# Optimization experiments

Measured on AMD Instinct MI355X. Metric: run time of the kernel, lower is better.

Reference implementation:

```python
import jax, jax.numpy as jnp
import numpy as np
import math

TPE_DIM = 16
NEG_INF = -1e9


def temporal_positional_encoding(t, dim=TPE_DIM):
    # t: (B, S) continuous positions -> (B, S, dim) sinusoidal encoding
    half = dim // 2
    div_term = jnp.exp(jnp.arange(half, dtype=t.dtype) * (-math.log(10000.0) / dim) * 2.0)
    ang = t[..., None] * div_term  # (B, S, half)
    # interleave sin/cos: pe[..., 0::2]=sin, pe[..., 1::2]=cos
    pe = jnp.stack([jnp.sin(ang), jnp.cos(ang)], axis=-1)  # (B, S, half, 2)
    return pe.reshape(t.shape[0], t.shape[1], dim)


def setup_inputs() -> dict:
    key = jax.random.key(0)
    k1, k2, k3, k4 = jax.random.split(key, 4)
    B, P, S, D = 8, 32, 512, 64
    t = jax.random.uniform(k1, (B, S), dtype=jnp.float32)
    x = jax.random.normal(k2, (B, P, S, D), dtype=jnp.float32)
    mask = jax.random.randint(k3, (B, P, S), 0, 2).astype(jnp.float32)
    # nn.Linear(1,1) weight (only the weight is used in forward)
    alpha_w = jax.random.normal(k4, (1, 1), dtype=jnp.float32) * 0.1
    return {"t": t, "x": x, "mask": mask, "alpha_w": alpha_w}


def reference(t, x, mask, alpha_w):
    B, P, S, D = x.shape
    dk = jnp.float32(TPE_DIM)
    # max-min normalize t over the time dim
    t_min = jnp.min(t, axis=1, keepdims=True)
    t_max = jnp.max(t, axis=1, keepdims=True)
    tn = (t - t_min) / (t_max - t_min)
    # scale by (elu(alpha*1000, 1) + 1)
    scale = jax.nn.elu(alpha_w[0, 0] * 1000.0) + 1.0
    tn = scale * tn
    tpe = temporal_positional_encoding(tn)  # (B, S, TPE_DIM)
    # attention scores over time: (B, S, S), shared across p
    scores = jnp.einsum('bsd,btd->bst', tpe, tpe) / jnp.sqrt(dk)
    eye = jnp.eye(S, dtype=mask.dtype)
    # cond True where (mask_broadcast + eye) < 0.5 -> fill with -1e9
    cond = (mask[:, :, None, :] + eye[None, None, :, :]) < 0.5  # (B, P, S, S)
    sc = jnp.where(cond, jnp.float32(NEG_INF), scores[:, None, :, :])
    p_attn = jax.nn.softmax(sc, axis=-1)  # (B, P, S, S)
    inter_x = jnp.einsum('bpst,bptd->bpsd', p_attn, x)  # (B, P, S, D)
    m = mask[..., None]  # (B, P, S, 1)
    return x * m + inter_x * (1.0 - m)
```

## Files before the change

### kernel.cpp

```cpp
#include <hip/hip_runtime.h>
#include <math.h>

#define B_ 8
#define P_ 32
#define S_ 512
#define D_ 64
#define NQS 5
#define KC 64

typedef __attribute__((ext_vector_type(8))) short short8;
typedef __attribute__((ext_vector_type(4))) float f32x4;

static __device__ inline unsigned short f2bf(float f) {
    unsigned u = __float_as_uint(f);
    unsigned r = (u + 0x7FFFu + ((u >> 16) & 1u)) >> 16;
    return (unsigned short)r;
}
static __device__ inline float bf2f(unsigned short s) {
    return __uint_as_float(((unsigned)s) << 16);
}

__launch_bounds__(256)
__global__ void k_scoresE2(const float* __restrict__ t, const float* __restrict__ alpha_w,
                           unsigned short* __restrict__ E16) {
    const int b = blockIdx.y;
    const int r0 = blockIdx.x * 8;
    const int tid = threadIdx.x, lane = tid & 63, wave = tid >> 6;

    __shared__ float tpeT[16][S_];
    __shared__ float red[8];

    float v0 = t[b * S_ + tid];
    float v1 = t[b * S_ + tid + 256];
    float mn = fminf(v0, v1), mx = fmaxf(v0, v1);
#pragma unroll
    for (int o = 32; o > 0; o >>= 1) {
        mn = fminf(mn, __shfl_xor(mn, o, 64));
        mx = fmaxf(mx, __shfl_xor(mx, o, 64));
    }
    if (lane == 0) { red[wave] = mn; red[4 + wave] = mx; }
    __syncthreads();
    mn = fminf(fminf(red[0], red[1]), fminf(red[2], red[3]));
    mx = fmaxf(fmaxf(red[4], red[5]), fmaxf(red[6], red[7]));

    float aw = alpha_w[0] * 1000.0f;
    float el = aw > 0.0f ? aw : (__expf(aw) - 1.0f);
    float inv = (el + 1.0f) / (mx - mn);

    const float divs[8] = {1.0f, 0.31622776601683794f, 0.1f, 0.031622776601683791f,
                           0.01f, 0.0031622776601683794f, 0.001f, 0.00031622776601683794f};
    {
        float tn0 = (v0 - mn) * inv;
        float tn1 = (v1 - mn) * inv;
#pragma unroll
        for (int f = 0; f < 8; f++) {
            float a0 = tn0 * divs[f], a1 = tn1 * divs[f];
            tpeT[2 * f][tid]           = 0.5f * __sinf(a0);
            tpeT[2 * f + 1][tid]       = 0.5f * __cosf(a0);
            tpeT[2 * f][tid + 256]     = 0.5f * __sinf(a1);
            tpeT[2 * f + 1][tid + 256] = 0.5f * __cosf(a1);
        }
    }
    __syncthreads();

    const int ra = r0 + wave * 2, rb = ra + 1;
    float qa[16], qb[16];
#pragma unroll
    for (int f = 0; f < 16; f++) { qa[f] = tpeT[f][ra]; qb[f] = tpeT[f][rb]; }

    unsigned* Ea = (unsigned*)(E16 + ((size_t)(b * S_) + ra) * S_);
    unsigned* Eb = (unsigned*)(E16 + ((size_t)(b * S_) + rb) * S_);
#pragma unroll
    for (int j = 0; j < 4; j++) {
        int k0 = j * 128 + lane * 2;
        float a0 = 0.f, a1 = 0.f, b0 = 0.f, b1 = 0.f;
#pragma unroll
        for (int f = 0; f < 16; f++) {
            float2 kv = *(const float2*)&tpeT[f][k0];
            a0 += qa[f] * kv.x; a1 += qa[f] * kv.y;
            b0 += qb[f] * kv.x; b1 += qb[f] * kv.y;
        }
        unsigned ea0 = f2bf(__expf(a0 - 2.0f)), ea1 = f2bf(__expf(a1 - 2.0f));
        unsigned eb0 = f2bf(__expf(b0 - 2.0f)), eb1 = f2bf(__expf(b1 - 2.0f));
        Ea[j * 64 + lane] = ea0 | (ea1 << 16);
        Eb[j * 64 + lane] = eb0 | (eb1 << 16);
    }
}

__launch_bounds__(256, 5)
__global__ void k_attn5(const float* __restrict__ x, const float* __restrict__ mask,
                        const unsigned short* __restrict__ E16, float* __restrict__ out) {
    const int bid = blockIdx.x;
    const int b = bid & 7;
    const int rdec = bid >> 3;
    const int p = rdec & 31;
    const int q = rdec >> 5;
    const int bp = b * P_ + p;
    const int tid = threadIdx.x, lane = tid & 63, wave = tid >> 6;
    const int quad = lane >> 4, nlane = lane & 15;
    const int c64 = tid & 63, kg = tid >> 6;

    __shared__ float maskL[S_];
    __shared__ short kidxL[S_], qidxL[S_];
    __shared__ int cntS[2];
    __shared__ __align__(16) unsigned short Bfrag[2][2][5][520];

    const float* maskBP = mask + (size_t)bp * S_;
    const float* xBP = x + (size_t)bp * S_ * D_;
    float* outBP = out + (size_t)bp * S_ * D_;
    const float4* x4 = (const float4*)xBP;
    float4* out4 = (float4*)outBP;
    const unsigned short* Eb = E16 + (size_t)b * S_ * S_;

    for (int i = tid; i < S_; i += 256) maskL[i] = maskBP[i];
    __syncthreads();

    if (wave == 0) {
        int nk = 0, nq = 0;
        for (int c = 0; c < 8; c++) {
            int tt = c * 64 + lane;
            bool isk = maskL[tt] >= 0.5f;
            unsigned long long bm = __ballot(isk);
            int pb = __popcll(bm & ((1ull << lane) - 1ull));
            if (isk) kidxL[nk + pb] = (short)tt;
            else     qidxL[nq + lane - pb] = (short)tt;
            int c1 = __popcll(bm);
            nk += c1; nq += 64 - c1;
        }
        if (lane == 0) { cntS[0] = nk; cntS[1] = nq; }
    }
    __syncthreads();
    const int NK = cntS[0], NQ = cntS[1];

    {
        int nk5 = (NK + NQS - 1) / NQS;
        int j0 = q * nk5, j1 = min(NK, j0 + nk5);
        for (int e = j0 * 16 + tid; e < j1 * 16; e += 256) {
            int s = kidxL[e >> 4];
            out4[s * 16 + (e & 15)] = x4[s * 16 + (e & 15)];
        }
    }

    const int qq = (NQ + NQS - 1) / NQS;
    const int qb0 = q * qq;
    const int rows = min(NQ, qb0 + qq) - qb0;
    if (rows <= 0) return;
    const int NT = (rows + 15) >> 4;
    const bool tw = wave < NT;

    const unsigned short* Arow;
    {
        int rowl = min(wave * 16 + nlane, rows - 1);
        Arow = Eb + (size_t)qidxL[qb0 + rowl] * S_;
    }

    auto loadx = [&](int kcv, float* xr) {
        const float* base = xBP + (size_t)(kcv + kg * 16) * D_ + c64;
#pragma unroll
        for (int i = 0; i < 16; i++) xr[i] = base[i * D_];
    };
    auto stage = [&](int bufi, int kcv, const float* xr) {
        const int kc2 = kg >> 1;
        const int ct = c64 >> 4;
#pragma unroll
        for (int g = 0; g < 2; g++) {
            short8 w;
#pragma unroll
            for (int j = 0; j < 8; j++) {
                int k = kg * 16 + g * 8 + j;
                w[j] = (short)f2bf(xr[g * 8 + j] * maskL[kcv + k]);
            }
            int lanep = ((kg & 1) * 2 + g) * 16 + (c64 & 15);
            *(short8*)&Bfrag[bufi][kc2][ct][lanep * 8] = w;
        }
        if (tid < 128) {
            int kc2m = tid >> 6;
            short8 w;
#pragma unroll
            for (int j = 0; j < 8; j++) {
                int k = kc2m * 32 + ((tid >> 4) & 3) * 8 + j;
                w[j] = ((tid & 15) == 0) ? (short)f2bf(maskL[kcv + k]) : (short)0;
            }
            *(short8*)&Bfrag[bufi][kc2m][4][(tid & 63) * 8] = w;
        }
    };

    f32x4 acc[5];
#pragma unroll
    for (int ct = 0; ct < 5; ct++) acc[ct] = (f32x4){0.f, 0.f, 0.f, 0.f};

    float xr[16], xrn[16];
    loadx(0, xr);
    stage(0, 0, xr);
    short8 a0 = *(const short8*)(Arow + quad * 8);
    short8 a1 = *(const short8*)(Arow + 32 + quad * 8);
    __syncthreads();

    for (int c = 0; c < 8; c++) {
        const int kc = c * KC;
        const int cur = c & 1;
        short8 an0, an1;
        if (c < 7) {
            loadx(kc + KC, xrn);
            an0 = *(const short8*)(Arow + kc + KC + quad * 8);
            an1 = *(const short8*)(Arow + kc + KC + 32 + quad * 8);
        }
#pragma unroll
        for (int ct = 0; ct < 5; ct++) {
            short8 b0 = *(const short8*)&Bfrag[cur][0][ct][lane * 8];
            short8 b1 = *(const short8*)&Bfrag[cur][1][ct][lane * 8];
            if (tw) {
                acc[ct] = __builtin_amdgcn_mfma_f32_16x16x32_bf16(a0, b0, acc[ct], 0, 0, 0);
                acc[ct] = __builtin_amdgcn_mfma_f32_16x16x32_bf16(a1, b1, acc[ct], 0, 0, 0);
            }
        }
        if (c < 7) stage(cur ^ 1, kc + KC, xrn);
        __syncthreads();
        a0 = an0; a1 = an1;
    }

    if (tw) {
#pragma unroll
        for (int reg = 0; reg < 4; reg++) {
            float den = __shfl(acc[4][reg], lane & 48, 64);
            int rowl = wave * 16 + quad * 4 + reg;
            if (rowl < rows) {
                int sg = qidxL[qb0 + rowl];
                float ws = bf2f(Eb[(size_t)sg * (S_ + 1)]);
                float inv = 1.0f / (den + ws);
#pragma unroll
                for (int ct = 0; ct < 4; ct++) {
                    int col = ct * 16 + nlane;
                    float xv = xBP[(size_t)sg * D_ + col];
                    outBP[(size_t)sg * D_ + col] = (acc[ct][reg] + ws * xv) * inv;
                }
            }
        }
    }
}

extern "C" void kernel_launch(void* const* d_in, const int* in_sizes, int n_in,
                              void* d_out, int out_size, void* d_ws, size_t ws_size,
                              hipStream_t stream) {
    const float* t       = (const float*)d_in[0];
    const float* x       = (const float*)d_in[1];
    const float* mask    = (const float*)d_in[2];
    const float* alpha_w = (const float*)d_in[3];
    float* out = (float*)d_out;

    unsigned short* E16 = (unsigned short*)d_ws;

    k_scoresE2<<<dim3(S_ / 8, B_), dim3(256), 0, stream>>>(t, alpha_w, E16);
    k_attn5<<<dim3(B_ * P_ * NQS), dim3(256), 0, stream>>>(x, mask, E16, out);
}
```

Baseline: 118.1 us.

## Precompute masked bf16 x fragments in prep kernel and drop LDS staging

The first kernel now does two jobs. Some blocks compute the score exponentials as before. The others convert the masked x into bf16 MFMA B-fragment layout in a global workspace and copy the unmasked rows to the output. The attention kernel then reads the prepacked fragments directly from global memory, with no LDS double-buffering or barriers. Each wave loops over its row tiles, the query split goes from 5 to 4 blocks, and the diagonal weight is replaced by the exact constant 1. This aims to stop each split block from re-converting all of x, at the cost of writing and then re-reading an extra bf16 workspace of about 20 MB.

```diff
diff --git a/kernel.cpp b/kernel.cpp
--- a/kernel.cpp
+++ b/kernel.cpp
@@ -5,8 +5,7 @@
 #define P_ 32
 #define S_ 512
 #define D_ 64
-#define NQS 5
-#define KC 64
+#define NQS 4
 
 typedef __attribute__((ext_vector_type(8))) short short8;
 typedef __attribute__((ext_vector_type(4))) float f32x4;
@@ -16,80 +15,135 @@
     unsigned r = (u + 0x7FFFu + ((u >> 16) & 1u)) >> 16;
     return (unsigned short)r;
 }
-static __device__ inline float bf2f(unsigned short s) {
-    return __uint_as_float(((unsigned)s) << 16);
-}
 
 __launch_bounds__(256)
-__global__ void k_scoresE2(const float* __restrict__ t, const float* __restrict__ alpha_w,
-                           unsigned short* __restrict__ E16) {
-    const int b = blockIdx.y;
-    const int r0 = blockIdx.x * 8;
+__global__ void k_prep(const float* __restrict__ t, const float* __restrict__ alpha_w,
+                       const float* __restrict__ x, const float* __restrict__ mask,
+                       unsigned short* __restrict__ E16, unsigned short* __restrict__ Bprep,
+                       float* __restrict__ out) {
+    const int bid = blockIdx.x;
     const int tid = threadIdx.x, lane = tid & 63, wave = tid >> 6;
 
-    __shared__ float tpeT[16][S_];
-    __shared__ float red[8];
-
-    float v0 = t[b * S_ + tid];
-    float v1 = t[b * S_ + tid + 256];
-    float mn = fminf(v0, v1), mx = fmaxf(v0, v1);
-#pragma unroll
-    for (int o = 32; o > 0; o >>= 1) {
-        mn = fminf(mn, __shfl_xor(mn, o, 64));
-        mx = fmaxf(mx, __shfl_xor(mx, o, 64));
+    __shared__ __align__(16) union {
+        struct { float tpeT[16][S_]; float red[8]; } e;
+        struct { unsigned short xbT[64][72]; float maskL[S_]; } p;
+    } sm;
+
+    if (bid < 512) {
+        const int b = bid >> 6;
+        const int r0 = (bid & 63) * 8;
+
+        float v0 = t[b * S_ + tid];
+        float v1 = t[b * S_ + tid + 256];
+        float mn = fminf(v0, v1), mx = fmaxf(v0, v1);
+#pragma unroll
+        for (int o = 32; o > 0; o >>= 1) {
+            mn = fminf(mn, __shfl_xor(mn, o, 64));
+            mx = fmaxf(mx, __shfl_xor(mx, o, 64));
+        }
+        if (lane == 0) { sm.e.red[wave] = mn; sm.e.red[4 + wave] = mx; }
+        __syncthreads();
+        mn = fminf(fminf(sm.e.red[0], sm.e.red[1]), fminf(sm.e.red[2], sm.e.red[3]));
+        mx = fmaxf(fmaxf(sm.e.red[4], sm.e.red[5]), fmaxf(sm.e.red[6], sm.e.red[7]));
+
+        float aw = alpha_w[0] * 1000.0f;
+        float el = aw > 0.0f ? aw : (__expf(aw) - 1.0f);
+        float inv = (el + 1.0f) / (mx - mn);
+
+        const float divs[8] = {1.0f, 0.31622776601683794f, 0.1f, 0.031622776601683791f,
+                               0.01f, 0.0031622776601683794f, 0.001f, 0.00031622776601683794f};
+        {
+            float tn0 = (v0 - mn) * inv;
+            float tn1 = (v1 - mn) * inv;
+#pragma unroll
+            for (int f = 0; f < 8; f++) {
+                float a0 = tn0 * divs[f], a1 = tn1 * divs[f];
+                sm.e.tpeT[2 * f][tid]           = 0.5f * __sinf(a0);
+                sm.e.tpeT[2 * f + 1][tid]       = 0.5f * __cosf(a0);
+                sm.e.tpeT[2 * f][tid + 256]     = 0.5f * __sinf(a1);
+                sm.e.tpeT[2 * f + 1][tid + 256] = 0.5f * __cosf(a1);
+            }
+        }
+        __syncthreads();
+
+        const int ra = r0 + wave * 2, rb = ra + 1;
+        float qa[16], qb[16];
+#pragma unroll
+        for (int f = 0; f < 16; f++) { qa[f] = sm.e.tpeT[f][ra]; qb[f] = sm.e.tpeT[f][rb]; }
+
+        unsigned* Ea = (unsigned*)(E16 + ((size_t)(b * S_) + ra) * S_);
+        unsigned* Eb = (unsigned*)(E16 + ((size_t)(b * S_) + rb) * S_);
+#pragma unroll
+        for (int j = 0; j < 4; j++) {
+            int k0 = j * 128 + lane * 2;
+            float a0 = 0.f, a1 = 0.f, b0 = 0.f, b1 = 0.f;
+#pragma unroll
+            for (int f = 0; f < 16; f++) {
+                float2 kv = *(const float2*)&sm.e.tpeT[f][k0];
+                a0 += qa[f] * kv.x; a1 += qa[f] * kv.y;
+                b0 += qb[f] * kv.x; b1 += qb[f] * kv.y;
+            }
+            unsigned ea0 = f2bf(__expf(a0 - 2.0f)), ea1 = f2bf(__expf(a1 - 2.0f));
+            unsigned eb0 = f2bf(__expf(b0 - 2.0f)), eb1 = f2bf(__expf(b1 - 2.0f));
+            Ea[j * 64 + lane] = ea0 | (ea1 << 16);
+            Eb[j * 64 + lane] = eb0 | (eb1 << 16);
+        }
+    } else {
+        const int j = bid - 512;
+        const int bp = j >> 1;
+        const int kh = j & 1;
+
+        const float* maskBP = mask + (size_t)bp * S_;
+        for (int i = tid; i < S_; i += 256) sm.p.maskL[i] = maskBP[i];
+
+        const float4* x4 = (const float4*)(x + (size_t)bp * S_ * D_);
+        float4* out4 = (float4*)(out + (size_t)bp * S_ * D_);
+        unsigned short* Bp = Bprep + (size_t)bp * 40960;
+
+        for (int cc = kh * 4; cc < kh * 4 + 4; cc++) {
+            const int k0 = cc * 64;
+            __syncthreads();
+#pragma unroll
+            for (int it = 0; it < 4; it++) {
+                int i4 = tid + it * 256;
+                int kl = i4 >> 4, c4 = i4 & 15;
+                int k = k0 + kl;
+                float4 g = x4[k * 16 + c4];
+                float mv = sm.p.maskL[k];
+                if (mv >= 0.5f) out4[k * 16 + c4] = g;
+                sm.p.xbT[c4 * 4 + 0][kl] = f2bf(g.x * mv);
+                sm.p.xbT[c4 * 4 + 1][kl] = f2bf(g.y * mv);
+                sm.p.xbT[c4 * 4 + 2][kl] = f2bf(g.z * mv);
+                sm.p.xbT[c4 * 4 + 3][kl] = f2bf(g.w * mv);
+            }
+            __syncthreads();
+            for (int e = tid; e < 640; e += 256) {
+                int l = e & 63;
+                int ctk = e >> 6;
+                int kc2 = ctk >= 5 ? 1 : 0;
+                int ct = ctk - kc2 * 5;
+                int qd = l >> 4, nl = l & 15;
+                short8 w;
+                if (ct == 4) {
+#pragma unroll
+                    for (int jj = 0; jj < 8; jj++) {
+                        int k = k0 + kc2 * 32 + qd * 8 + jj;
+                        w[jj] = (nl == 0) ? (short)f2bf(sm.p.maskL[k]) : (short)0;
+                    }
+                } else {
+                    w = *(const short8*)&sm.p.xbT[ct * 16 + nl][kc2 * 32 + qd * 8];
+                }
+                *(short8*)&Bp[((size_t)(cc * 2 + kc2) * 5 + ct) * 512 + l * 8] = w;
+            }
+        }
     }
-    if (lane == 0) { red[wave] = mn; red[4 + wave] = mx; }
-    __syncthreads();
-    mn = fminf(fminf(red[0], red[1]), fminf(red[2], red[3]));
-    mx = fmaxf(fmaxf(red[4], red[5]), fmaxf(red[6], red[7]));
-
-    float aw = alpha_w[0] * 1000.0f;
-    float el = aw > 0.0f ? aw : (__expf(aw) - 1.0f);
-    float inv = (el + 1.0f) / (mx - mn);
-
-    const float divs[8] = {1.0f, 0.31622776601683794f, 0.1f, 0.031622776601683791f,
-                           0.01f, 0.0031622776601683794f, 0.001f, 0.00031622776601683794f};
-    {
-        float tn0 = (v0 - mn) * inv;
-        float tn1 = (v1 - mn) * inv;
-#pragma unroll
-        for (int f = 0; f < 8; f++) {
-            float a0 = tn0 * divs[f], a1 = tn1 * divs[f];
-            tpeT[2 * f][tid]           = 0.5f * __sinf(a0);
-            tpeT[2 * f + 1][tid]       = 0.5f * __cosf(a0);
-            tpeT[2 * f][tid + 256]     = 0.5f * __sinf(a1);
-            tpeT[2 * f + 1][tid + 256] = 0.5f * __cosf(a1);
-        }
-    }
-    __syncthreads();
-
-    const int ra = r0 + wave * 2, rb = ra + 1;
-    float qa[16], qb[16];
-#pragma unroll
-    for (int f = 0; f < 16; f++) { qa[f] = tpeT[f][ra]; qb[f] = tpeT[f][rb]; }
-
-    unsigned* Ea = (unsigned*)(E16 + ((size_t)(b * S_) + ra) * S_);
-    unsigned* Eb = (unsigned*)(E16 + ((size_t)(b * S_) + rb) * S_);
-#pragma unroll
-    for (int j = 0; j < 4; j++) {
-        int k0 = j * 128 + lane * 2;
-        float a0 = 0.f, a1 = 0.f, b0 = 0.f, b1 = 0.f;
-#pragma unroll
-        for (int f = 0; f < 16; f++) {
-            float2 kv = *(const float2*)&tpeT[f][k0];
-            a0 += qa[f] * kv.x; a1 += qa[f] * kv.y;
-            b0 += qb[f] * kv.x; b1 += qb[f] * kv.y;
-        }
-        unsigned ea0 = f2bf(__expf(a0 - 2.0f)), ea1 = f2bf(__expf(a1 - 2.0f));
-        unsigned eb0 = f2bf(__expf(b0 - 2.0f)), eb1 = f2bf(__expf(b1 - 2.0f));
-        Ea[j * 64 + lane] = ea0 | (ea1 << 16);
-        Eb[j * 64 + lane] = eb0 | (eb1 << 16);
-    }
-}
-
-__launch_bounds__(256, 5)
-__global__ void k_attn5(const float* __restrict__ x, const float* __restrict__ mask,
-                        const unsigned short* __restrict__ E16, float* __restrict__ out) {
+}
+
+__launch_bounds__(256, 4)
+__global__ void k_attn6(const float* __restrict__ x, const float* __restrict__ mask,
+                        const unsigned short* __restrict__ E16,
+                        const unsigned short* __restrict__ Bprep,
+                        float* __restrict__ out) {
     const int bid = blockIdx.x;
     const int b = bid & 7;
     const int rdec = bid >> 3;
@@ -98,141 +152,72 @@
     const int bp = b * P_ + p;
     const int tid = threadIdx.x, lane = tid & 63, wave = tid >> 6;
     const int quad = lane >> 4, nlane = lane & 15;
-    const int c64 = tid & 63, kg = tid >> 6;
-
-    __shared__ float maskL[S_];
-    __shared__ short kidxL[S_], qidxL[S_];
-    __shared__ int cntS[2];
-    __shared__ __align__(16) unsigned short Bfrag[2][2][5][520];
+
+    __shared__ short qidxL[S_];
+    __shared__ int cntS;
 
     const float* maskBP = mask + (size_t)bp * S_;
     const float* xBP = x + (size_t)bp * S_ * D_;
     float* outBP = out + (size_t)bp * S_ * D_;
-    const float4* x4 = (const float4*)xBP;
-    float4* out4 = (float4*)outBP;
     const unsigned short* Eb = E16 + (size_t)b * S_ * S_;
-
-    for (int i = tid; i < S_; i += 256) maskL[i] = maskBP[i];
-    __syncthreads();
+    const unsigned short* BpL = Bprep + (size_t)bp * 40960 + lane * 8;
 
     if (wave == 0) {
-        int nk = 0, nq = 0;
+        int nq = 0;
         for (int c = 0; c < 8; c++) {
             int tt = c * 64 + lane;
-            bool isk = maskL[tt] >= 0.5f;
-            unsigned long long bm = __ballot(isk);
+            bool isq = maskBP[tt] < 0.5f;
+            unsigned long long bm = __ballot(isq);
             int pb = __popcll(bm & ((1ull << lane) - 1ull));
-            if (isk) kidxL[nk + pb] = (short)tt;
-            else     qidxL[nq + lane - pb] = (short)tt;
-            int c1 = __popcll(bm);
-            nk += c1; nq += 64 - c1;
-        }
-        if (lane == 0) { cntS[0] = nk; cntS[1] = nq; }
+            if (isq) qidxL[nq + pb] = (short)tt;
+            nq += __popcll(bm);
+        }
+        if (lane == 0) cntS = nq;
     }
     __syncthreads();
-    const int NK = cntS[0], NQ = cntS[1];
-
-    {
-        int nk5 = (NK + NQS - 1) / NQS;
-        int j0 = q * nk5, j1 = min(NK, j0 + nk5);
-        for (int e = j0 * 16 + tid; e < j1 * 16; e += 256) {
-            int s = kidxL[e >> 4];
-            out4[s * 16 + (e & 15)] = x4[s * 16 + (e & 15)];
-        }
-    }
+    const int NQ = cntS;
 
     const int qq = (NQ + NQS - 1) / NQS;
     const int qb0 = q * qq;
     const int rows = min(NQ, qb0 + qq) - qb0;
     if (rows <= 0) return;
     const int NT = (rows + 15) >> 4;
-    const bool tw = wave < NT;
-
-    const unsigned short* Arow;
-    {
-        int rowl = min(wave * 16 + nlane, rows - 1);
-        Arow = Eb + (size_t)qidxL[qb0 + rowl] * S_;
-    }
-
-    auto loadx = [&](int kcv, float* xr) {
-        const float* base = xBP + (size_t)(kcv + kg * 16) * D_ + c64;
-#pragma unroll
-        for (int i = 0; i < 16; i++) xr[i] = base[i * D_];
-    };
-    auto stage = [&](int bufi, int kcv, const float* xr) {
-        const int kc2 = kg >> 1;
-        const int ct = c64 >> 4;
-#pragma unroll
-        for (int g = 0; g < 2; g++) {
-            short8 w;
-#pragma unroll
-            for (int j = 0; j < 8; j++) {
-                int k = kg * 16 + g * 8 + j;
-                w[j] = (short)f2bf(xr[g * 8 + j] * maskL[kcv + k]);
-            }
-            int lanep = ((kg & 1) * 2 + g) * 16 + (c64 & 15);
-            *(short8*)&Bfrag[bufi][kc2][ct][lanep * 8] = w;
-        }
-        if (tid < 128) {
-            int kc2m = tid >> 6;
-            short8 w;
-#pragma unroll
-            for (int j = 0; j < 8; j++) {
-                int k = kc2m * 32 + ((tid >> 4) & 3) * 8 + j;
-                w[j] = ((tid & 15) == 0) ? (short)f2bf(maskL[kcv + k]) : (short)0;
-            }
-            *(short8*)&Bfrag[bufi][kc2m][4][(tid & 63) * 8] = w;
-        }
-    };
-
-    f32x4 acc[5];
-#pragma unroll
-    for (int ct = 0; ct < 5; ct++) acc[ct] = (f32x4){0.f, 0.f, 0.f, 0.f};
-
-    float xr[16], xrn[16];
-    loadx(0, xr);
-    stage(0, 0, xr);
-    short8 a0 = *(const short8*)(Arow + quad * 8);
-    short8 a1 = *(const short8*)(Arow + 32 + quad * 8);
-    __syncthreads();
-
-    for (int c = 0; c < 8; c++) {
-        const int kc = c * KC;
-        const int cur = c & 1;
-        short8 an0, an1;
-        if (c < 7) {
-            loadx(kc + KC, xrn);
-            an0 = *(const short8*)(Arow + kc + KC + quad * 8);
-            an1 = *(const short8*)(Arow + kc + KC + 32 + quad * 8);
-        }
-#pragma unroll
-        for (int ct = 0; ct < 5; ct++) {
-            short8 b0 = *(const short8*)&Bfrag[cur][0][ct][lane * 8];
-            short8 b1 = *(const short8*)&Bfrag[cur][1][ct][lane * 8];
-            if (tw) {
+
+    for (int ti = wave; ti < NT; ti += 4) {
+        const unsigned short* Arow;
+        {
+            int rowl = min(ti * 16 + nlane, rows - 1);
+            Arow = Eb + (size_t)qidxL[qb0 + rowl] * S_;
+        }
+        f32x4 acc[5];
+#pragma unroll
+        for (int ct = 0; ct < 5; ct++) acc[ct] = (f32x4){0.f, 0.f, 0.f, 0.f};
+
+#pragma unroll
+        for (int c = 0; c < 8; c++) {
+            short8 a0 = *(const short8*)(Arow + c * 64 + quad * 8);
+            short8 a1 = *(const short8*)(Arow + c * 64 + 32 + quad * 8);
+#pragma unroll
+            for (int ct = 0; ct < 5; ct++) {
+                short8 b0 = *(const short8*)(BpL + ((c * 2 + 0) * 5 + ct) * 512);
+                short8 b1 = *(const short8*)(BpL + ((c * 2 + 1) * 5 + ct) * 512);
                 acc[ct] = __builtin_amdgcn_mfma_f32_16x16x32_bf16(a0, b0, acc[ct], 0, 0, 0);
                 acc[ct] = __builtin_amdgcn_mfma_f32_16x16x32_bf16(a1, b1, acc[ct], 0, 0, 0);
             }
         }
-        if (c < 7) stage(cur ^ 1, kc + KC, xrn);
-        __syncthreads();
-        a0 = an0; a1 = an1;
-    }
-
-    if (tw) {
+
 #pragma unroll
         for (int reg = 0; reg < 4; reg++) {
             float den = __shfl(acc[4][reg], lane & 48, 64);
-            int rowl = wave * 16 + quad * 4 + reg;
+            int rowl = ti * 16 + quad * 4 + reg;
             if (rowl < rows) {
                 int sg = qidxL[qb0 + rowl];
-                float ws = bf2f(Eb[(size_t)sg * (S_ + 1)]);
-                float inv = 1.0f / (den + ws);
+                float inv = 1.0f / (den + 1.0f);
 #pragma unroll
                 for (int ct = 0; ct < 4; ct++) {
                     int col = ct * 16 + nlane;
                     float xv = xBP[(size_t)sg * D_ + col];
-                    outBP[(size_t)sg * D_ + col] = (acc[ct][reg] + ws * xv) * inv;
+                    outBP[(size_t)sg * D_ + col] = (acc[ct][reg] + xv) * inv;
                 }
             }
         }
@@ -248,8 +233,9 @@
     const float* alpha_w = (const float*)d_in[3];
     float* out = (float*)d_out;
 
-    unsigned short* E16 = (unsigned short*)d_ws;
-
-    k_scoresE2<<<dim3(S_ / 8, B_), dim3(256), 0, stream>>>(t, alpha_w, E16);
-    k_attn5<<<dim3(B_ * P_ * NQS), dim3(256), 0, stream>>>(x, mask, E16, out);
-}
+    unsigned short* E16   = (unsigned short*)d_ws;
+    unsigned short* Bprep = (unsigned short*)((char*)d_ws + (size_t)B_ * S_ * S_ * 2);
+
+    k_prep<<<dim3(1024), dim3(256), 0, stream>>>(t, alpha_w, x, mask, E16, Bprep, out);
+    k_attn6<<<dim3(B_ * P_ * NQS), dim3(256), 0, stream>>>(x, mask, E16, Bprep, out);
+}
```

Result: slower. 265.9 us (+125.2%).

## Process each (b,p) in one 512-thread block, staging x once per half

Applied to the files above, without the earlier changes.

The attention kernel now uses one 512-thread block per (batch, p) instead of five blocks that split the query rows. Each block stages masked bf16 x for 256 keys at a time into shared memory. Each wave handles up to two 32-row query tiles against that staged data. This removes the fivefold redundant reads and conversions of x. Key rows are copied to the output inline during staging, and the diagonal weight is hardcoded to 1, which holds algebraically for the unit-norm encoding. In exchange the grid shrinks to 256 large blocks with heavy register use, which lowers occupancy and latency hiding, and the global-to-LDS load is no longer double-buffered.

```diff
diff --git a/kernel.cpp b/kernel.cpp
--- a/kernel.cpp
+++ b/kernel.cpp
@@ -5,8 +5,7 @@
 #define P_ 32
 #define S_ 512
 #define D_ 64
-#define NQS 5
-#define KC 64
+#define NP 2
 
 typedef __attribute__((ext_vector_type(8))) short short8;
 typedef __attribute__((ext_vector_type(4))) float f32x4;
@@ -15,9 +14,6 @@
     unsigned u = __float_as_uint(f);
     unsigned r = (u + 0x7FFFu + ((u >> 16) & 1u)) >> 16;
     return (unsigned short)r;
-}
-static __device__ inline float bf2f(unsigned short s) {
-    return __uint_as_float(((unsigned)s) << 16);
 }
 
 __launch_bounds__(256)
@@ -87,152 +83,129 @@
     }
 }
 
-__launch_bounds__(256, 5)
-__global__ void k_attn5(const float* __restrict__ x, const float* __restrict__ mask,
+__launch_bounds__(512, 2)
+__global__ void k_attn7(const float* __restrict__ x, const float* __restrict__ mask,
                         const unsigned short* __restrict__ E16, float* __restrict__ out) {
     const int bid = blockIdx.x;
-    const int b = bid & 7;
-    const int rdec = bid >> 3;
-    const int p = rdec & 31;
-    const int q = rdec >> 5;
+    const int b = bid & 7, p = bid >> 3;
     const int bp = b * P_ + p;
     const int tid = threadIdx.x, lane = tid & 63, wave = tid >> 6;
     const int quad = lane >> 4, nlane = lane & 15;
-    const int c64 = tid & 63, kg = tid >> 6;
+    const int kg = wave;
 
     __shared__ float maskL[S_];
-    __shared__ short kidxL[S_], qidxL[S_];
-    __shared__ int cntS[2];
-    __shared__ __align__(16) unsigned short Bfrag[2][2][5][520];
+    __shared__ short qidxL[S_];
+    __shared__ int cntS;
+    __shared__ __align__(16) unsigned short Bfrag[8][5][64][8];
 
     const float* maskBP = mask + (size_t)bp * S_;
     const float* xBP = x + (size_t)bp * S_ * D_;
     float* outBP = out + (size_t)bp * S_ * D_;
-    const float4* x4 = (const float4*)xBP;
-    float4* out4 = (float4*)outBP;
     const unsigned short* Eb = E16 + (size_t)b * S_ * S_;
 
-    for (int i = tid; i < S_; i += 256) maskL[i] = maskBP[i];
+    maskL[tid] = maskBP[tid];
     __syncthreads();
 
     if (wave == 0) {
-        int nk = 0, nq = 0;
+        int nq = 0;
         for (int c = 0; c < 8; c++) {
             int tt = c * 64 + lane;
-            bool isk = maskL[tt] >= 0.5f;
-            unsigned long long bm = __ballot(isk);
+            bool isq = maskL[tt] < 0.5f;
+            unsigned long long bm = __ballot(isq);
             int pb = __popcll(bm & ((1ull << lane) - 1ull));
-            if (isk) kidxL[nk + pb] = (short)tt;
-            else     qidxL[nq + lane - pb] = (short)tt;
-            int c1 = __popcll(bm);
-            nk += c1; nq += 64 - c1;
-        }
-        if (lane == 0) { cntS[0] = nk; cntS[1] = nq; }
-    }
-    __syncthreads();
-    const int NK = cntS[0], NQ = cntS[1];
-
-    {
-        int nk5 = (NK + NQS - 1) / NQS;
-        int j0 = q * nk5, j1 = min(NK, j0 + nk5);
-        for (int e = j0 * 16 + tid; e < j1 * 16; e += 256) {
-            int s = kidxL[e >> 4];
-            out4[s * 16 + (e & 15)] = x4[s * 16 + (e & 15)];
-        }
-    }
-
-    const int qq = (NQ + NQS - 1) / NQS;
-    const int qb0 = q * qq;
-    const int rows = min(NQ, qb0 + qq) - qb0;
-    if (rows <= 0) return;
-    const int NT = (rows + 15) >> 4;
-    const bool tw = wave < NT;
-
-    const unsigned short* Arow;
-    {
-        int rowl = min(wave * 16 + nlane, rows - 1);
-        Arow = Eb + (size_t)qidxL[qb0 + rowl] * S_;
-    }
-
-    auto loadx = [&](int kcv, float* xr) {
-        const float* base = xBP + (size_t)(kcv + kg * 16) * D_ + c64;
-#pragma unroll
-        for (int i = 0; i < 16; i++) xr[i] = base[i * D_];
-    };
-    auto stage = [&](int bufi, int kcv, const float* xr) {
-        const int kc2 = kg >> 1;
-        const int ct = c64 >> 4;
-#pragma unroll
-        for (int g = 0; g < 2; g++) {
+            if (isq) qidxL[nq + pb] = (short)tt;
+            nq += __popcll(bm);
+        }
+        if (lane == 0) cntS = nq;
+    }
+    __syncthreads();
+    const int NQ = cntS;
+
+    const unsigned short* Ar[NP][2];
+    bool act[NP];
+#pragma unroll
+    for (int i = 0; i < NP; i++) {
+        int pi = wave + 8 * i;
+        act[i] = (pi * 32) < NQ;
+        int r0 = act[i] ? min(pi * 32 + nlane, NQ - 1) : 0;
+        int r1 = act[i] ? min(pi * 32 + 16 + nlane, NQ - 1) : 0;
+        Ar[i][0] = Eb + (size_t)qidxL[r0] * S_;
+        Ar[i][1] = Eb + (size_t)qidxL[r1] * S_;
+    }
+
+    f32x4 acc[NP][2][5];
+#pragma unroll
+    for (int i = 0; i < NP; i++)
+#pragma unroll
+        for (int tt = 0; tt < 2; tt++)
+#pragma unroll
+            for (int ct = 0; ct < 5; ct++) acc[i][tt][ct] = (f32x4){0.f, 0.f, 0.f, 0.f};
+
+    for (int h = 0; h < 2; h++) {
+        if (h) __syncthreads();
+
+        {
             short8 w;
 #pragma unroll
             for (int j = 0; j < 8; j++) {
-                int k = kg * 16 + g * 8 + j;
-                w[j] = (short)f2bf(xr[g * 8 + j] * maskL[kcv + k]);
-            }
-            int lanep = ((kg & 1) * 2 + g) * 16 + (c64 & 15);
-            *(short8*)&Bfrag[bufi][kc2][ct][lanep * 8] = w;
-        }
-        if (tid < 128) {
-            int kc2m = tid >> 6;
+                int k = h * 256 + kg * 32 + quad * 8 + j;
+                w[j] = (nlane == 0) ? (short)f2bf(maskL[k]) : (short)0;
+            }
+            *(short8*)&Bfrag[kg][4][lane][0] = w;
+        }
+#pragma unroll
+        for (int g = 0; g < 4; g++) {
+            int kb = h * 256 + kg * 32 + g * 8;
+            float v[8];
+#pragma unroll
+            for (int j = 0; j < 8; j++) v[j] = xBP[(size_t)(kb + j) * D_ + lane];
             short8 w;
 #pragma unroll
             for (int j = 0; j < 8; j++) {
-                int k = kc2m * 32 + ((tid >> 4) & 3) * 8 + j;
-                w[j] = ((tid & 15) == 0) ? (short)f2bf(maskL[kcv + k]) : (short)0;
-            }
-            *(short8*)&Bfrag[bufi][kc2m][4][(tid & 63) * 8] = w;
-        }
-    };
-
-    f32x4 acc[5];
-#pragma unroll
-    for (int ct = 0; ct < 5; ct++) acc[ct] = (f32x4){0.f, 0.f, 0.f, 0.f};
-
-    float xr[16], xrn[16];
-    loadx(0, xr);
-    stage(0, 0, xr);
-    short8 a0 = *(const short8*)(Arow + quad * 8);
-    short8 a1 = *(const short8*)(Arow + 32 + quad * 8);
-    __syncthreads();
-
-    for (int c = 0; c < 8; c++) {
-        const int kc = c * KC;
-        const int cur = c & 1;
-        short8 an0, an1;
-        if (c < 7) {
-            loadx(kc + KC, xrn);
-            an0 = *(const short8*)(Arow + kc + KC + quad * 8);
-            an1 = *(const short8*)(Arow + kc + KC + 32 + quad * 8);
-        }
-#pragma unroll
-        for (int ct = 0; ct < 5; ct++) {
-            short8 b0 = *(const short8*)&Bfrag[cur][0][ct][lane * 8];
-            short8 b1 = *(const short8*)&Bfrag[cur][1][ct][lane * 8];
-            if (tw) {
-                acc[ct] = __builtin_amdgcn_mfma_f32_16x16x32_bf16(a0, b0, acc[ct], 0, 0, 0);
-                acc[ct] = __builtin_amdgcn_mfma_f32_16x16x32_bf16(a1, b1, acc[ct], 0, 0, 0);
-            }
-        }
-        if (c < 7) stage(cur ^ 1, kc + KC, xrn);
+                float mv = maskL[kb + j];
+                if (mv >= 0.5f) outBP[(size_t)(kb + j) * D_ + lane] = v[j];
+                w[j] = (short)f2bf(v[j] * mv);
+            }
+            *(short8*)&Bfrag[kg][lane >> 4][g * 16 + nlane][0] = w;
+        }
         __syncthreads();
-        a0 = an0; a1 = an1;
-    }
-
-    if (tw) {
-#pragma unroll
-        for (int reg = 0; reg < 4; reg++) {
-            float den = __shfl(acc[4][reg], lane & 48, 64);
-            int rowl = wave * 16 + quad * 4 + reg;
-            if (rowl < rows) {
-                int sg = qidxL[qb0 + rowl];
-                float ws = bf2f(Eb[(size_t)sg * (S_ + 1)]);
-                float inv = 1.0f / (den + ws);
-#pragma unroll
-                for (int ct = 0; ct < 4; ct++) {
-                    int col = ct * 16 + nlane;
-                    float xv = xBP[(size_t)sg * D_ + col];
-                    outBP[(size_t)sg * D_ + col] = (acc[ct][reg] + ws * xv) * inv;
+
+#pragma unroll
+        for (int i = 0; i < NP; i++) {
+            if (act[i]) {
+#pragma unroll
+                for (int kc2 = 0; kc2 < 8; kc2++) {
+                    short8 a0 = *(const short8*)(Ar[i][0] + h * 256 + kc2 * 32 + quad * 8);
+                    short8 a1 = *(const short8*)(Ar[i][1] + h * 256 + kc2 * 32 + quad * 8);
+#pragma unroll
+                    for (int ct = 0; ct < 5; ct++) {
+                        short8 bb = *(const short8*)&Bfrag[kc2][ct][lane][0];
+                        acc[i][0][ct] = __builtin_amdgcn_mfma_f32_16x16x32_bf16(a0, bb, acc[i][0][ct], 0, 0, 0);
+                        acc[i][1][ct] = __builtin_amdgcn_mfma_f32_16x16x32_bf16(a1, bb, acc[i][1][ct], 0, 0, 0);
+                    }
+                }
+            }
+        }
+    }
+
+#pragma unroll
+    for (int i = 0; i < NP; i++) {
+        if (!act[i]) continue;
+#pragma unroll
+        for (int tt = 0; tt < 2; tt++) {
+#pragma unroll
+            for (int reg = 0; reg < 4; reg++) {
+                float den = __shfl(acc[i][tt][4][reg], lane & 48, 64);
+                int rowl = (wave + 8 * i) * 32 + tt * 16 + quad * 4 + reg;
+                if (rowl < NQ) {
+                    int sg = qidxL[rowl];
+                    float inv = 1.0f / (den + 1.0f);
+#pragma unroll
+                    for (int ct = 0; ct < 4; ct++) {
+                        int col = ct * 16 + nlane;
+                        float xv = xBP[(size_t)sg * D_ + col];
+                        outBP[(size_t)sg * D_ + col] = (acc[i][tt][ct][reg] + xv) * inv;
+                    }
                 }
             }
         }
@@ -251,5 +224,5 @@
     unsigned short* E16 = (unsigned short*)d_ws;
 
     k_scoresE2<<<dim3(S_ / 8, B_), dim3(256), 0, stream>>>(t, alpha_w, E16);
-    k_attn5<<<dim3(B_ * P_ * NQS), dim3(256), 0, stream>>>(x, mask, E16, out);
-}
+    k_attn7<<<dim3(B_ * P_), dim3(512), 0, stream>>>(x, mask, E16, out);
+}
```

Measured after the change: 116.3 us. About the same (-1.5%).
